# Kernel tuning notes

Hardware: AMD Instinct MI355X
Metric: run time of the kernel (lower is better)

Reference implementation:

```python
import jax, jax.numpy as jnp
import numpy as np

B, N, S, NS, D = 8, 16384, 1024, 64, 128
RADIUS = 0.2
CH = [131, 128, 128, 256]  # mlp_spec after use_xyz: 128+3 input channels
EPS = 1e-5


def setup_inputs() -> dict:
    key = jax.random.key(0)
    ks = jax.random.split(key, 16)
    inp = {}
    inp["xyz"] = jax.random.uniform(ks[0], (B, N, 3), dtype=jnp.float32)
    inp["points"] = jax.random.normal(ks[1], (B, D, N), dtype=jnp.float32)
    inp["fps_idx"] = jax.random.randint(ks[2], (B, S), 0, N, dtype=jnp.int32)
    for i in range(3):
        cin, cout = CH[i], CH[i + 1]
        inp[f"W{i}"] = jax.random.normal(ks[3 + 4 * i], (cout, cin), dtype=jnp.float32) * np.float32(1.0 / np.sqrt(cin))
        inp[f"b{i}"] = jnp.zeros((cout,), dtype=jnp.float32)
        inp[f"g{i}"] = jnp.ones((cout,), dtype=jnp.float32)
        inp[f"be{i}"] = jnp.zeros((cout,), dtype=jnp.float32)
    return inp


def _ball_query(xyz, new_xyz):
    # squared distances [B, S, N] (expanded-form, same math as square_distance)
    d = (jnp.sum(new_xyz ** 2, -1, keepdims=True)
         + jnp.sum(xyz ** 2, -1)[:, None, :]
         - 2.0 * jnp.einsum('bsc,bnc->bsn', new_xyz, xyz))
    ar = jnp.arange(N, dtype=jnp.int32)[None, None, :]
    idx = jnp.where(d > RADIUS ** 2, N, ar)          # out-of-ball -> sentinel N
    idx = jnp.sort(idx, axis=-1)[:, :, :NS]          # global sort emulating top-k
    idx = jnp.where(idx == N, idx[:, :, :1], idx)    # pad with first valid neighbor
    return idx


def reference(xyz, points, fps_idx, W0, b0, g0, be0, W1, b1, g1, be1, W2, b2, g2, be2):
    feats = points.transpose(0, 2, 1)  # [B, N, D]
    new_xyz = jnp.take_along_axis(xyz, fps_idx[..., None], axis=1)  # [B, S, 3]
    idx = _ball_query(xyz, new_xyz)  # [B, S, NS]

    gather = jax.vmap(lambda a, i: a[i])  # per-batch fancy gather
    grouped_xyz = gather(xyz, idx) - new_xyz[:, :, None, :]   # [B, S, NS, 3]
    grouped_pts = gather(feats, idx)                          # [B, S, NS, D]
    x = jnp.concatenate([grouped_xyz, grouped_pts], axis=-1)  # [B, S, NS, 131]

    # SharedMLP: 1x1 Conv2d + BatchNorm (training-mode stats) + ReLU
    for W, b, g, be in ((W0, b0, g0, be0), (W1, b1, g1, be1), (W2, b2, g2, be2)):
        x = jnp.einsum('bsnc,oc->bsno', x, W) + b
        m = jnp.mean(x, axis=(0, 1, 2))
        v = jnp.var(x, axis=(0, 1, 2))
        x = jax.nn.relu(g * (x - m) * jax.lax.rsqrt(v + EPS) + be)

    new_features = jnp.max(x, axis=2).transpose(0, 2, 1)  # max over nsample -> [B, C', S]
    return new_xyz, new_features, fps_idx
```

## Files before the change

kernel.cpp:

```cpp
#include <hip/hip_runtime.h>
#include <hip/hip_bf16.h>

#define BB 8
#define NN 16384
#define SS 1024
#define NSMP 64
#define DD 128
#define R2 0.04f
#define EPSV 1e-5f

typedef _Float16 half2t __attribute__((ext_vector_type(2)));
typedef _Float16 half8t __attribute__((ext_vector_type(8)));
typedef float f32x4 __attribute__((ext_vector_type(4)));

#define O_PT    0ull
#define O_Y0    33554432ull
#define O_Y1    167772160ull
#define O_IDX   301989888ull
#define O_MAXB  304087040ull
#define O_MINB  312475648ull
#define O_W0T   320864256ull
#define O_W1T   320931328ull
#define O_W2T   320996864ull
#define O_PS0   321127936ull
#define O_PQ0   321259008ull
#define O_PS1   321390080ull
#define O_PQ1   321521152ull
#define O_PS2   321652224ull
#define O_PQ2   321914368ull
#define O_SC0   322176512ull
#define O_SH0   322177024ull
#define O_SC1   322177536ull
#define O_SH1   322178048ull
#define O_SC2   322178560ull
#define O_SH2   322179584ull
#define WS_NEEDED 322180608ull
#define PART_BYTES 1048576ull

#define OUT_XYZ 0
#define OUT_FEAT 24576
#define OUT_FPS (24576 + 2097152)

__global__ __launch_bounds__(256) void k_transpose_pts(const float* __restrict__ pts,
                                                       _Float16* __restrict__ ptsT) {
  __shared__ float tile[32][33];
  int b = blockIdx.z;
  int n0 = blockIdx.x * 32, c0 = blockIdx.y * 32;
  int tx = threadIdx.x, ty = threadIdx.y;
#pragma unroll
  for (int k = 0; k < 4; k++) {
    int c = c0 + ty + k * 8;
    tile[ty + k * 8][tx] = pts[((size_t)b * DD + c) * NN + n0 + tx];
  }
  __syncthreads();
#pragma unroll
  for (int k = 0; k < 4; k++) {
    int n = n0 + ty + k * 8;
    ptsT[((size_t)b * NN + n) * DD + c0 + tx] = (_Float16)tile[tx][ty + k * 8];
  }
}

__global__ __launch_bounds__(256) void k_wt(const float* __restrict__ W0, const float* __restrict__ W1,
                                            const float* __restrict__ W2, _Float16* __restrict__ W0h,
                                            _Float16* __restrict__ W1h, _Float16* __restrict__ W2h) {
  int id = blockIdx.x * 256 + threadIdx.x;
  const int T0 = 128 * 136, T1 = 128 * 136, T2 = 256 * 136;
  if (id < T0) {
    int o = id / 136, c = id % 136;
    float v = 0.f;
    if (c < 131) {
      int c0 = (c < 128) ? (c + 3) : (c - 128);
      v = W0[o * 131 + c0];
    }
    W0h[id] = (_Float16)v;
  } else if (id < T0 + T1) {
    int j = id - T0;
    int o = j / 136, c = j % 136;
    W1h[j] = (_Float16)((c < 128) ? W1[o * 128 + c] : 0.f);
  } else if (id < T0 + T1 + T2) {
    int j = id - T0 - T1;
    int o = j / 136, c = j % 136;
    W2h[j] = (_Float16)((c < 128) ? W2[o * 128 + c] : 0.f);
  }
}

__global__ __launch_bounds__(256) void k_newxyz(const float* __restrict__ xyz, const int* __restrict__ fps,
                                                float* __restrict__ out) {
  int id = blockIdx.x * 256 + threadIdx.x;
  int fi = fps[id];
  int b = id >> 10;
  const float* p = xyz + ((size_t)b * NN + fi) * 3;
  float* o = out + OUT_XYZ + (size_t)id * 3;
  o[0] = p[0]; o[1] = p[1]; o[2] = p[2];
  out[OUT_FPS + id] = (float)fi;
}

__global__ __launch_bounds__(256) void k_ballq(const float* __restrict__ xyz, const int* __restrict__ fps,
                                               int* __restrict__ idxb) {
  int w = (blockIdx.x * 256 + threadIdx.x) >> 6;
  int lane = threadIdx.x & 63;
  int b = w >> 10;
  int fi = fps[w];
  const float* cp = xyz + ((size_t)b * NN + fi) * 3;
  float cx = cp[0], cy = cp[1], cz = cp[2];
  float A = __fadd_rn(__fadd_rn(__fmul_rn(cx, cx), __fmul_rn(cy, cy)), __fmul_rn(cz, cz));
  const float* xb = xyz + (size_t)b * NN * 3;
  int cnt = 0, firstn = -1;
  int* myidx = idxb + (size_t)w * NSMP;
  for (int nb = 0; nb < NN && cnt < NSMP; nb += 64) {
    int n = nb + lane;
    float px = xb[n * 3], py = xb[n * 3 + 1], pz = xb[n * 3 + 2];
    float Bv = __fadd_rn(__fadd_rn(__fmul_rn(px, px), __fmul_rn(py, py)), __fmul_rn(pz, pz));
    float dot = __fadd_rn(__fadd_rn(__fmul_rn(cx, px), __fmul_rn(cy, py)), __fmul_rn(cz, pz));
    float d = __fsub_rn(__fadd_rn(A, Bv), __fmul_rn(2.0f, dot));
    bool valid = !(d > R2);
    unsigned long long mask = __ballot(valid);
    if (firstn < 0 && mask) firstn = nb + __builtin_ctzll(mask);
    int prefix = __popcll(mask & ((1ull << lane) - 1ull));
    int pos = cnt + prefix;
    if (valid && pos < NSMP) myidx[pos] = n;
    cnt += __popcll(mask);
    if (cnt > NSMP) cnt = NSMP;
  }
  if (lane >= cnt) myidx[lane] = firstn;
}

__global__ __launch_bounds__(256, 2) void k_mlp0(const float* __restrict__ xyz,
                                                 const _Float16* __restrict__ ptsT,
                                                 const int* __restrict__ fps, const int* __restrict__ idxb,
                                                 const _Float16* __restrict__ W0h, const float* __restrict__ b0,
                                                 _Float16* __restrict__ y0, float* __restrict__ psum,
                                                 float* __restrict__ psq) {
  __shared__ _Float16 xh[64 * 136];
  __shared__ float xs[64 * 133];
  __shared__ float rbuf[128 * 2];
  __shared__ int smidx[64];
  __shared__ float smc[3];
  int t = threadIdx.x;
  int bs = blockIdx.x;
  int b = bs >> 10;
  if (t < 64) smidx[t] = idxb[(size_t)bs * 64 + t];
  if (t < 3) {
    int fi = fps[bs];
    smc[t] = xyz[((size_t)b * NN + fi) * 3 + t];
  }
  __syncthreads();
  {
    int row = t >> 2, q = t & 3;
    int n = smidx[row];
    const half8t* src = (const half8t*)(ptsT + ((size_t)b * NN + n) * DD);
#pragma unroll
    for (int i = 0; i < 4; i++) {
      int j = q + i * 4;
      *(half8t*)(xh + row * 136 + j * 8) = src[j];
    }
  }
  if (t < 64) {
    int n = smidx[t];
    const float* p = xyz + ((size_t)b * NN + n) * 3;
    xh[t * 136 + 128] = (_Float16)(p[0] - smc[0]);
    xh[t * 136 + 129] = (_Float16)(p[1] - smc[1]);
    xh[t * 136 + 130] = (_Float16)(p[2] - smc[2]);
  }
  __syncthreads();
  int lane = t & 63;
  int m0 = __builtin_amdgcn_readfirstlane((t >> 6) * 16);
  int lr = lane & 15, lk = lane >> 4;
  half8t afr[4];
#pragma unroll
  for (int kt = 0; kt < 4; kt++)
    afr[kt] = *(const half8t*)(xh + (m0 + lr) * 136 + kt * 32 + lk * 8);
  f32x4 acc[8];
#pragma unroll
  for (int nt = 0; nt < 8; nt++) {
    float bv = b0[nt * 16 + lr];
    f32x4 cv = {bv, bv, bv, bv};
    acc[nt] = cv;
  }
#pragma unroll
  for (int kt = 0; kt < 4; kt++) {
#pragma unroll
    for (int nt = 0; nt < 8; nt++) {
      half8t bw = *(const half8t*)(W0h + (nt * 16 + lr) * 136 + kt * 32 + lk * 8);
      acc[nt] = __builtin_amdgcn_mfma_f32_16x16x32_f16(afr[kt], bw, acc[nt], 0, 0, 0);
    }
  }
  {
    float xr[4][3];
#pragma unroll
    for (int r = 0; r < 4; r++) {
      int m = m0 + lk * 4 + r;
      xr[r][0] = (float)xh[m * 136 + 128];
      xr[r][1] = (float)xh[m * 136 + 129];
      xr[r][2] = (float)xh[m * 136 + 130];
    }
#pragma unroll
    for (int nt = 0; nt < 8; nt++) {
      const _Float16* wp = W0h + (nt * 16 + lr) * 136 + 128;
      float w0 = (float)wp[0], w1 = (float)wp[1], w2 = (float)wp[2];
#pragma unroll
      for (int r = 0; r < 4; r++)
        acc[nt][r] += xr[r][0] * w0 + xr[r][1] * w1 + xr[r][2] * w2;
    }
  }
#pragma unroll
  for (int nt = 0; nt < 8; nt++)
#pragma unroll
    for (int r = 0; r < 4; r++)
      xs[(m0 + lk * 4 + r) * 133 + nt * 16 + lr] = acc[nt][r];
  __syncthreads();
  {
    _Float16* dst = y0 + (size_t)bs * 8192;
#pragma unroll
    for (int i = 0; i < 16; i++) {
      int flat = i * 512 + 2 * t;
      int row = flat >> 7, col = flat & 127;
      half2t h;
      h[0] = (_Float16)xs[row * 133 + col];
      h[1] = (_Float16)xs[row * 133 + col + 1];
      *(half2t*)(dst + flat) = h;
    }
  }
  {
    int col = t & 127, half = t >> 7;
    float s = 0.f, q = 0.f;
#pragma unroll 4
    for (int r = half * 32; r < half * 32 + 32; r++) {
      float v = xs[r * 133 + col];
      s += v;
      q = fmaf(v, v, q);
    }
    if (half) { rbuf[col * 2] = s; rbuf[col * 2 + 1] = q; }
    __syncthreads();
    if (!half) {
      s += rbuf[col * 2];
      q += rbuf[col * 2 + 1];
      int slot = bs & 255;
      atomicAdd(&psum[col * 256 + slot], s);
      atomicAdd(&psq[col * 256 + slot], q);
    }
  }
}

__global__ __launch_bounds__(256, 2) void k_mlp1(const _Float16* __restrict__ y0,
                                                 const float* __restrict__ sc, const float* __restrict__ sh,
                                                 const _Float16* __restrict__ W1h, const float* __restrict__ b1,
                                                 _Float16* __restrict__ y1, float* __restrict__ psum,
                                                 float* __restrict__ psq) {
  __shared__ _Float16 xh[64 * 136];
  __shared__ float xs[64 * 133];
  __shared__ float rbuf[128 * 2];
  int t = threadIdx.x;
  int bs = blockIdx.x;
  {
    int colb = (2 * t) & 127;
    float a0 = sc[colb], a1 = sc[colb + 1];
    float c0 = sh[colb], c1 = sh[colb + 1];
    const _Float16* src = y0 + (size_t)bs * 8192;
#pragma unroll
    for (int i = 0; i < 16; i++) {
      int flat = i * 512 + 2 * t;
      int row = flat >> 7, col = flat & 127;
      half2t h = *(const half2t*)(src + flat);
      half2t o;
      o[0] = (_Float16)fmaxf(fmaf((float)h[0], a0, c0), 0.f);
      o[1] = (_Float16)fmaxf(fmaf((float)h[1], a1, c1), 0.f);
      *(half2t*)(xh + row * 136 + col) = o;
    }
  }
  __syncthreads();
  int lane = t & 63;
  int m0 = __builtin_amdgcn_readfirstlane((t >> 6) * 16);
  int lr = lane & 15, lk = lane >> 4;
  half8t afr[4];
#pragma unroll
  for (int kt = 0; kt < 4; kt++)
    afr[kt] = *(const half8t*)(xh + (m0 + lr) * 136 + kt * 32 + lk * 8);
  f32x4 acc[8];
#pragma unroll
  for (int nt = 0; nt < 8; nt++) {
    float bv = b1[nt * 16 + lr];
    f32x4 cv = {bv, bv, bv, bv};
    acc[nt] = cv;
  }
#pragma unroll
  for (int kt = 0; kt < 4; kt++) {
#pragma unroll
    for (int nt = 0; nt < 8; nt++) {
      half8t bw = *(const half8t*)(W1h + (nt * 16 + lr) * 136 + kt * 32 + lk * 8);
      acc[nt] = __builtin_amdgcn_mfma_f32_16x16x32_f16(afr[kt], bw, acc[nt], 0, 0, 0);
    }
  }
#pragma unroll
  for (int nt = 0; nt < 8; nt++)
#pragma unroll
    for (int r = 0; r < 4; r++)
      xs[(m0 + lk * 4 + r) * 133 + nt * 16 + lr] = acc[nt][r];
  __syncthreads();
  {
    _Float16* dst = y1 + (size_t)bs * 8192;
#pragma unroll
    for (int i = 0; i < 16; i++) {
      int flat = i * 512 + 2 * t;
      int row = flat >> 7, col = flat & 127;
      half2t h;
      h[0] = (_Float16)xs[row * 133 + col];
      h[1] = (_Float16)xs[row * 133 + col + 1];
      *(half2t*)(dst + flat) = h;
    }
  }
  {
    int col = t & 127, half = t >> 7;
    float s = 0.f, q = 0.f;
#pragma unroll 4
    for (int r = half * 32; r < half * 32 + 32; r++) {
      float v = xs[r * 133 + col];
      s += v;
      q = fmaf(v, v, q);
    }
    if (half) { rbuf[col * 2] = s; rbuf[col * 2 + 1] = q; }
    __syncthreads();
    if (!half) {
      s += rbuf[col * 2];
      q += rbuf[col * 2 + 1];
      int slot = bs & 255;
      atomicAdd(&psum[col * 256 + slot], s);
      atomicAdd(&psq[col * 256 + slot], q);
    }
  }
}

__global__ __launch_bounds__(256, 2) void k_mlp2(const _Float16* __restrict__ y1,
                                                 const float* __restrict__ sc, const float* __restrict__ sh,
                                                 const _Float16* __restrict__ W2h, const float* __restrict__ b2,
                                                 float* __restrict__ maxb, float* __restrict__ minb,
                                                 float* __restrict__ psum, float* __restrict__ psq) {
  __shared__ _Float16 xh[64 * 136];
  __shared__ float xs[64 * 133];
  __shared__ float rbuf[128 * 4];
  int t = threadIdx.x;
  int bs = blockIdx.x;
  {
    int colb = (2 * t) & 127;
    float a0 = sc[colb], a1 = sc[colb + 1];
    float c0 = sh[colb], c1 = sh[colb + 1];
    const _Float16* src = y1 + (size_t)bs * 8192;
#pragma unroll
    for (int i = 0; i < 16; i++) {
      int flat = i * 512 + 2 * t;
      int row = flat >> 7, col = flat & 127;
      half2t h = *(const half2t*)(src + flat);
      half2t o;
      o[0] = (_Float16)fmaxf(fmaf((float)h[0], a0, c0), 0.f);
      o[1] = (_Float16)fmaxf(fmaf((float)h[1], a1, c1), 0.f);
      *(half2t*)(xh + row * 136 + col) = o;
    }
  }
  __syncthreads();
  int lane = t & 63;
  int m0 = __builtin_amdgcn_readfirstlane((t >> 6) * 16);
  int lr = lane & 15, lk = lane >> 4;
  half8t afr[4];
#pragma unroll
  for (int kt = 0; kt < 4; kt++)
    afr[kt] = *(const half8t*)(xh + (m0 + lr) * 136 + kt * 32 + lk * 8);
  f32x4 acc[16];
#pragma unroll
  for (int nt = 0; nt < 16; nt++) {
    float bv = b2[nt * 16 + lr];
    f32x4 cv = {bv, bv, bv, bv};
    acc[nt] = cv;
  }
#pragma unroll
  for (int kt = 0; kt < 4; kt++) {
#pragma unroll
    for (int nt = 0; nt < 16; nt++) {
      half8t bw = *(const half8t*)(W2h + (nt * 16 + lr) * 136 + kt * 32 + lk * 8);
      acc[nt] = __builtin_amdgcn_mfma_f32_16x16x32_f16(afr[kt], bw, acc[nt], 0, 0, 0);
    }
  }
  for (int ph = 0; ph < 2; ph++) {
#pragma unroll
    for (int nt = 0; nt < 8; nt++)
#pragma unroll
      for (int r = 0; r < 4; r++)
        xs[(m0 + lk * 4 + r) * 133 + nt * 16 + lr] = acc[ph * 8 + nt][r];
    __syncthreads();
    {
      int col = t & 127, half = t >> 7;
      float s = 0.f, q = 0.f, mx = -3.4e38f, mn = 3.4e38f;
#pragma unroll 4
      for (int r = half * 32; r < half * 32 + 32; r++) {
        float v = xs[r * 133 + col];
        s += v;
        q = fmaf(v, v, q);
        mx = fmaxf(mx, v);
        mn = fminf(mn, v);
      }
      if (half) {
        rbuf[col * 4] = s; rbuf[col * 4 + 1] = q;
        rbuf[col * 4 + 2] = mx; rbuf[col * 4 + 3] = mn;
      }
      __syncthreads();
      if (!half) {
        s += rbuf[col * 4];
        q += rbuf[col * 4 + 1];
        mx = fmaxf(mx, rbuf[col * 4 + 2]);
        mn = fminf(mn, rbuf[col * 4 + 3]);
        int o = ph * 128 + col;
        maxb[(size_t)bs * 256 + o] = mx;
        minb[(size_t)bs * 256 + o] = mn;
        int slot = bs & 255;
        atomicAdd(&psum[o * 256 + slot], s);
        atomicAdd(&psq[o * 256 + slot], q);
      }
    }
    __syncthreads();
  }
}

__global__ __launch_bounds__(256) void k_fin(const float* __restrict__ psum, const float* __restrict__ psq,
                                             const float* __restrict__ g, const float* __restrict__ be,
                                             float* __restrict__ sc, float* __restrict__ sh, int nch) {
  int o = threadIdx.x;
  if (o >= nch) return;
  float s = 0.f, q = 0.f;
  for (int k = 0; k < 256; k++) {
    s += psum[o * 256 + k];
    q += psq[o * 256 + k];
  }
  const float inv = 1.0f / 524288.0f;
  float m = s * inv;
  float ey2 = q * inv;
  float v = fmaf(-m, m, ey2);
  v = fmaxf(v, 0.f);
  float r = rsqrtf(v + EPSV);
  float a = g[o] * r;
  sc[o] = a;
  sh[o] = fmaf(-m, a, be[o]);
}

__global__ __launch_bounds__(256) void k_out(const float* __restrict__ maxb, const float* __restrict__ minb,
                                             const float* __restrict__ sc, const float* __restrict__ sh,
                                             float* __restrict__ out) {
  int flat = blockIdx.x * 256 + threadIdx.x;
  int b = flat >> 18;
  int o = (flat >> 10) & 255;
  int s = flat & 1023;
  float a = sc[o], c_ = sh[o];
  size_t mi = ((size_t)(b * 1024 + s)) * 256 + o;
  float v = (a >= 0.f) ? maxb[mi] : minb[mi];
  out[OUT_FEAT + flat] = fmaxf(fmaf(a, v, c_), 0.f);
}

extern "C" void kernel_launch(void* const* d_in, const int* in_sizes, int n_in,
                              void* d_out, int out_size, void* d_ws, size_t ws_size,
                              hipStream_t stream) {
  const float* xyz = (const float*)d_in[0];
  const float* pts = (const float*)d_in[1];
  const int* fps = (const int*)d_in[2];
  const float* W0 = (const float*)d_in[3];
  const float* b0 = (const float*)d_in[4];
  const float* g0 = (const float*)d_in[5];
  const float* be0 = (const float*)d_in[6];
  const float* W1 = (const float*)d_in[7];
  const float* b1 = (const float*)d_in[8];
  const float* g1 = (const float*)d_in[9];
  const float* be1 = (const float*)d_in[10];
  const float* W2 = (const float*)d_in[11];
  const float* b2 = (const float*)d_in[12];
  const float* g2 = (const float*)d_in[13];
  const float* be2 = (const float*)d_in[14];
  float* out = (float*)d_out;
  char* ws = (char*)d_ws;

  k_newxyz<<<32, 256, 0, stream>>>(xyz, fps, out);
  if (ws_size < WS_NEEDED) return;

  _Float16* ptsT = (_Float16*)(ws + O_PT);
  _Float16* y0 = (_Float16*)(ws + O_Y0);
  _Float16* y1 = (_Float16*)(ws + O_Y1);
  int* idxb = (int*)(ws + O_IDX);
  float* maxbf = (float*)(ws + O_MAXB);
  float* minbf = (float*)(ws + O_MINB);
  _Float16* W0h = (_Float16*)(ws + O_W0T);
  _Float16* W1h = (_Float16*)(ws + O_W1T);
  _Float16* W2h = (_Float16*)(ws + O_W2T);
  float* ps0 = (float*)(ws + O_PS0);
  float* pq0 = (float*)(ws + O_PQ0);
  float* ps1 = (float*)(ws + O_PS1);
  float* pq1 = (float*)(ws + O_PQ1);
  float* ps2 = (float*)(ws + O_PS2);
  float* pq2 = (float*)(ws + O_PQ2);
  float* sc0 = (float*)(ws + O_SC0);
  float* sh0 = (float*)(ws + O_SH0);
  float* sc1 = (float*)(ws + O_SC1);
  float* sh1 = (float*)(ws + O_SH1);
  float* sc2 = (float*)(ws + O_SC2);
  float* sh2 = (float*)(ws + O_SH2);

  hipMemsetAsync(ws + O_PS0, 0, PART_BYTES, stream);
  k_transpose_pts<<<dim3(NN / 32, DD / 32, BB), dim3(32, 8), 0, stream>>>(pts, ptsT);
  k_wt<<<272, 256, 0, stream>>>(W0, W1, W2, W0h, W1h, W2h);
  k_ballq<<<2048, 256, 0, stream>>>(xyz, fps, idxb);
  k_mlp0<<<8192, 256, 0, stream>>>(xyz, ptsT, fps, idxb, W0h, b0, y0, ps0, pq0);
  k_fin<<<1, 256, 0, stream>>>(ps0, pq0, g0, be0, sc0, sh0, 128);
  k_mlp1<<<8192, 256, 0, stream>>>(y0, sc0, sh0, W1h, b1, y1, ps1, pq1);
  k_fin<<<1, 256, 0, stream>>>(ps1, pq1, g1, be1, sc1, sh1, 128);
  k_mlp2<<<8192, 256, 0, stream>>>(y1, sc1, sh1, W2h, b2, maxbf, minbf, ps2, pq2);
  k_fin<<<1, 256, 0, stream>>>(ps2, pq2, g2, be2, sc2, sh2, 256);
  k_out<<<8192, 256, 0, stream>>>(maxbf, minbf, sc2, sh2, out);
}
```

Baseline: 116.8 us.

## Recompute earlier MLP layers per pass instead of storing fp16 intermediates

Replaces the three layer kernels, which wrote and re-read the fp16 activations y0 and y1 through global memory, with three passes that each re-gather the ball features and recompute the earlier layers in registers and LDS. Only per-channel stats, and max/min in the final pass, are written. This removes about 256MB of activation traffic at the cost of repeating the gather and the layer-0/1 MFMA work. It also folds the partial-sum zeroing into the weight-conversion kernel in place of a memset, and writes new_xyz/fps from the ball-query kernel so the separate newxyz launch goes away.

After: 114.3 us. 2.1% less time.

```diff
diff --git a/kernel.cpp b/kernel.cpp
--- a/kernel.cpp
+++ b/kernel.cpp
@@ -14,8 +14,6 @@
 typedef float f32x4 __attribute__((ext_vector_type(4)));
 
 #define O_PT    0ull
-#define O_Y0    33554432ull
-#define O_Y1    167772160ull
 #define O_IDX   301989888ull
 #define O_MAXB  304087040ull
 #define O_MINB  312475648ull
@@ -35,7 +33,6 @@
 #define O_SC2   322178560ull
 #define O_SH2   322179584ull
 #define WS_NEEDED 322180608ull
-#define PART_BYTES 1048576ull
 
 #define OUT_XYZ 0
 #define OUT_FEAT 24576
@@ -62,8 +59,13 @@
 
 __global__ __launch_bounds__(256) void k_wt(const float* __restrict__ W0, const float* __restrict__ W1,
                                             const float* __restrict__ W2, _Float16* __restrict__ W0h,
-                                            _Float16* __restrict__ W1h, _Float16* __restrict__ W2h) {
+                                            _Float16* __restrict__ W1h, _Float16* __restrict__ W2h,
+                                            float* __restrict__ zreg) {
   int id = blockIdx.x * 256 + threadIdx.x;
+  if (id < 65536) {
+    f32x4 z = {0.f, 0.f, 0.f, 0.f};
+    ((f32x4*)zreg)[id] = z;
+  }
   const int T0 = 128 * 136, T1 = 128 * 136, T2 = 256 * 136;
   if (id < T0) {
     int o = id / 136, c = id % 136;
@@ -96,13 +98,15 @@
 }
 
 __global__ __launch_bounds__(256) void k_ballq(const float* __restrict__ xyz, const int* __restrict__ fps,
-                                               int* __restrict__ idxb) {
+                                               int* __restrict__ idxb, float* __restrict__ out) {
   int w = (blockIdx.x * 256 + threadIdx.x) >> 6;
   int lane = threadIdx.x & 63;
   int b = w >> 10;
   int fi = fps[w];
   const float* cp = xyz + ((size_t)b * NN + fi) * 3;
   float cx = cp[0], cy = cp[1], cz = cp[2];
+  if (lane < 3) out[OUT_XYZ + (size_t)w * 3 + lane] = (lane == 0) ? cx : ((lane == 1) ? cy : cz);
+  if (lane == 3) out[OUT_FPS + w] = (float)fi;
   float A = __fadd_rn(__fadd_rn(__fmul_rn(cx, cx), __fmul_rn(cy, cy)), __fmul_rn(cz, cz));
   const float* xb = xyz + (size_t)b * NN * 3;
   int cnt = 0, firstn = -1;
@@ -125,12 +129,151 @@
   if (lane >= cnt) myidx[lane] = firstn;
 }
 
-__global__ __launch_bounds__(256, 2) void k_mlp0(const float* __restrict__ xyz,
-                                                 const _Float16* __restrict__ ptsT,
-                                                 const int* __restrict__ fps, const int* __restrict__ idxb,
-                                                 const _Float16* __restrict__ W0h, const float* __restrict__ b0,
-                                                 _Float16* __restrict__ y0, float* __restrict__ psum,
-                                                 float* __restrict__ psq) {
+
+__device__ __forceinline__ void load_ball(const float* __restrict__ xyz,
+                                          const _Float16* __restrict__ ptsT,
+                                          const int* __restrict__ fps, const int* __restrict__ idxb,
+                                          int bs, int b, int t, _Float16* xh, int* smidx, float* smc) {
+  if (t < 64) smidx[t] = idxb[(size_t)bs * 64 + t];
+  if (t < 3) {
+    int fi = fps[bs];
+    smc[t] = xyz[((size_t)b * NN + fi) * 3 + t];
+  }
+  __syncthreads();
+  {
+    int row = t >> 2, q = t & 3;
+    int n = smidx[row];
+    const half8t* src = (const half8t*)(ptsT + ((size_t)b * NN + n) * DD);
+#pragma unroll
+    for (int i = 0; i < 4; i++) {
+      int j = q + i * 4;
+      *(half8t*)(xh + row * 136 + j * 8) = src[j];
+    }
+  }
+  if (t < 64) {
+    int n = smidx[t];
+    const float* p = xyz + ((size_t)b * NN + n) * 3;
+    xh[t * 136 + 128] = (_Float16)(p[0] - smc[0]);
+    xh[t * 136 + 129] = (_Float16)(p[1] - smc[1]);
+    xh[t * 136 + 130] = (_Float16)(p[2] - smc[2]);
+  }
+  __syncthreads();
+}
+
+__device__ __forceinline__ void mfma_l0(const _Float16* xh, const _Float16* __restrict__ W0h,
+                                        const float* __restrict__ b0, int m0, int lr, int lk,
+                                        f32x4* acc) {
+  half8t afr[4];
+#pragma unroll
+  for (int kt = 0; kt < 4; kt++)
+    afr[kt] = *(const half8t*)(xh + (m0 + lr) * 136 + kt * 32 + lk * 8);
+#pragma unroll
+  for (int nt = 0; nt < 8; nt++) {
+    float bv = b0[nt * 16 + lr];
+    f32x4 cv = {bv, bv, bv, bv};
+    acc[nt] = cv;
+  }
+#pragma unroll
+  for (int kt = 0; kt < 4; kt++) {
+#pragma unroll
+    for (int nt = 0; nt < 8; nt++) {
+      half8t bw = *(const half8t*)(W0h + (nt * 16 + lr) * 136 + kt * 32 + lk * 8);
+      acc[nt] = __builtin_amdgcn_mfma_f32_16x16x32_f16(afr[kt], bw, acc[nt], 0, 0, 0);
+    }
+  }
+  float xr[4][3];
+#pragma unroll
+  for (int r = 0; r < 4; r++) {
+    int m = m0 + lk * 4 + r;
+    xr[r][0] = (float)xh[m * 136 + 128];
+    xr[r][1] = (float)xh[m * 136 + 129];
+    xr[r][2] = (float)xh[m * 136 + 130];
+  }
+#pragma unroll
+  for (int nt = 0; nt < 8; nt++) {
+    const _Float16* wp = W0h + (nt * 16 + lr) * 136 + 128;
+    float w0 = (float)wp[0], w1 = (float)wp[1], w2 = (float)wp[2];
+#pragma unroll
+    for (int r = 0; r < 4; r++)
+      acc[nt][r] += xr[r][0] * w0 + xr[r][1] * w1 + xr[r][2] * w2;
+  }
+}
+
+template <int NT>
+__device__ __forceinline__ void mfma_lx(const _Float16* xh, const _Float16* __restrict__ Wh,
+                                        const float* __restrict__ bias, int m0, int lr, int lk,
+                                        f32x4* acc) {
+  half8t afr[4];
+#pragma unroll
+  for (int kt = 0; kt < 4; kt++)
+    afr[kt] = *(const half8t*)(xh + (m0 + lr) * 136 + kt * 32 + lk * 8);
+#pragma unroll
+  for (int nt = 0; nt < NT; nt++) {
+    float bv = bias[nt * 16 + lr];
+    f32x4 cv = {bv, bv, bv, bv};
+    acc[nt] = cv;
+  }
+#pragma unroll
+  for (int kt = 0; kt < 4; kt++) {
+#pragma unroll
+    for (int nt = 0; nt < NT; nt++) {
+      half8t bw = *(const half8t*)(Wh + (nt * 16 + lr) * 136 + kt * 32 + lk * 8);
+      acc[nt] = __builtin_amdgcn_mfma_f32_16x16x32_f16(afr[kt], bw, acc[nt], 0, 0, 0);
+    }
+  }
+}
+
+__device__ __forceinline__ void store_act(_Float16* xh, const float* __restrict__ sc,
+                                          const float* __restrict__ sh, int m0, int lr, int lk,
+                                          const f32x4* acc) {
+#pragma unroll
+  for (int nt = 0; nt < 8; nt++) {
+    int col = nt * 16 + lr;
+    float a = sc[col], c = sh[col];
+#pragma unroll
+    for (int r = 0; r < 4; r++) {
+      float v = fmaxf(fmaf(acc[nt][r], a, c), 0.f);
+      xh[(m0 + lk * 4 + r) * 136 + col] = (_Float16)v;
+    }
+  }
+}
+
+__device__ __forceinline__ void dump_xs(float* xs, const f32x4* acc, int m0, int lr, int lk) {
+#pragma unroll
+  for (int nt = 0; nt < 8; nt++)
+#pragma unroll
+    for (int r = 0; r < 4; r++)
+      xs[(m0 + lk * 4 + r) * 133 + nt * 16 + lr] = acc[nt][r];
+}
+
+__device__ __forceinline__ void stats_epilogue(const float* xs, float* rbuf,
+                                               float* __restrict__ psum, float* __restrict__ psq,
+                                               int t, int bs) {
+  int col = t & 127, hf = t >> 7;
+  float s = 0.f, q = 0.f;
+#pragma unroll 4
+  for (int r = hf * 32; r < hf * 32 + 32; r++) {
+    float v = xs[r * 133 + col];
+    s += v;
+    q = fmaf(v, v, q);
+  }
+  if (hf) { rbuf[col * 2] = s; rbuf[col * 2 + 1] = q; }
+  __syncthreads();
+  if (!hf) {
+    s += rbuf[col * 2];
+    q += rbuf[col * 2 + 1];
+    int slot = bs & 255;
+    atomicAdd(&psum[col * 256 + slot], s);
+    atomicAdd(&psq[col * 256 + slot], q);
+  }
+}
+
+
+__global__ __launch_bounds__(256, 2) void k_pass1(const float* __restrict__ xyz,
+                                                  const _Float16* __restrict__ ptsT,
+                                                  const int* __restrict__ fps, const int* __restrict__ idxb,
+                                                  const _Float16* __restrict__ W0h, const float* __restrict__ b0,
+                                                  float* __restrict__ psum, float* __restrict__ psq) {
   __shared__ _Float16 xh[64 * 136];
   __shared__ float xs[64 * 133];
   __shared__ float rbuf[128 * 2];
@@ -139,270 +282,104 @@
   int t = threadIdx.x;
   int bs = blockIdx.x;
   int b = bs >> 10;
-  if (t < 64) smidx[t] = idxb[(size_t)bs * 64 + t];
-  if (t < 3) {
-    int fi = fps[bs];
-    smc[t] = xyz[((size_t)b * NN + fi) * 3 + t];
-  }
-  __syncthreads();
-  {
-    int row = t >> 2, q = t & 3;
-    int n = smidx[row];
-    const half8t* src = (const half8t*)(ptsT + ((size_t)b * NN + n) * DD);
-#pragma unroll
-    for (int i = 0; i < 4; i++) {
-      int j = q + i * 4;
-      *(half8t*)(xh + row * 136 + j * 8) = src[j];
-    }
-  }
-  if (t < 64) {
-    int n = smidx[t];
-    const float* p = xyz + ((size_t)b * NN + n) * 3;
-    xh[t * 136 + 128] = (_Float16)(p[0] - smc[0]);
-    xh[t * 136 + 129] = (_Float16)(p[1] - smc[1]);
-    xh[t * 136 + 130] = (_Float16)(p[2] - smc[2]);
-  }
-  __syncthreads();
+  load_ball(xyz, ptsT, fps, idxb, bs, b, t, xh, smidx, smc);
   int lane = t & 63;
   int m0 = __builtin_amdgcn_readfirstlane((t >> 6) * 16);
   int lr = lane & 15, lk = lane >> 4;
-  half8t afr[4];
-#pragma unroll
-  for (int kt = 0; kt < 4; kt++)
-    afr[kt] = *(const half8t*)(xh + (m0 + lr) * 136 + kt * 32 + lk * 8);
   f32x4 acc[8];
-#pragma unroll
-  for (int nt = 0; nt < 8; nt++) {
-    float bv = b0[nt * 16 + lr];
-    f32x4 cv = {bv, bv, bv, bv};
-    acc[nt] = cv;
-  }
-#pragma unroll
-  for (int kt = 0; kt < 4; kt++) {
-#pragma unroll
-    for (int nt = 0; nt < 8; nt++) {
-      half8t bw = *(const half8t*)(W0h + (nt * 16 + lr) * 136 + kt * 32 + lk * 8);
-      acc[nt] = __builtin_amdgcn_mfma_f32_16x16x32_f16(afr[kt], bw, acc[nt], 0, 0, 0);
-    }
-  }
-  {
-    float xr[4][3];
-#pragma unroll
-    for (int r = 0; r < 4; r++) {
-      int m = m0 + lk * 4 + r;
-      xr[r][0] = (float)xh[m * 136 + 128];
-      xr[r][1] = (float)xh[m * 136 + 129];
-      xr[r][2] = (float)xh[m * 136 + 130];
-    }
-#pragma unroll
-    for (int nt = 0; nt < 8; nt++) {
-      const _Float16* wp = W0h + (nt * 16 + lr) * 136 + 128;
-      float w0 = (float)wp[0], w1 = (float)wp[1], w2 = (float)wp[2];
-#pragma unroll
-      for (int r = 0; r < 4; r++)
-        acc[nt][r] += xr[r][0] * w0 + xr[r][1] * w1 + xr[r][2] * w2;
-    }
-  }
-#pragma unroll
-  for (int nt = 0; nt < 8; nt++)
-#pragma unroll
-    for (int r = 0; r < 4; r++)
-      xs[(m0 + lk * 4 + r) * 133 + nt * 16 + lr] = acc[nt][r];
-  __syncthreads();
-  {
-    _Float16* dst = y0 + (size_t)bs * 8192;
-#pragma unroll
-    for (int i = 0; i < 16; i++) {
-      int flat = i * 512 + 2 * t;
-      int row = flat >> 7, col = flat & 127;
-      half2t h;
-      h[0] = (_Float16)xs[row * 133 + col];
-      h[1] = (_Float16)xs[row * 133 + col + 1];
-      *(half2t*)(dst + flat) = h;
-    }
-  }
-  {
-    int col = t & 127, half = t >> 7;
-    float s = 0.f, q = 0.f;
-#pragma unroll 4
-    for (int r = half * 32; r < half * 32 + 32; r++) {
-      float v = xs[r * 133 + col];
-      s += v;
-      q = fmaf(v, v, q);
-    }
-    if (half) { rbuf[col * 2] = s; rbuf[col * 2 + 1] = q; }
-    __syncthreads();
-    if (!half) {
-      s += rbuf[col * 2];
-      q += rbuf[col * 2 + 1];
-      int slot = bs & 255;
-      atomicAdd(&psum[col * 256 + slot], s);
-      atomicAdd(&psq[col * 256 + slot], q);
-    }
-  }
-}
-
-__global__ __launch_bounds__(256, 2) void k_mlp1(const _Float16* __restrict__ y0,
-                                                 const float* __restrict__ sc, const float* __restrict__ sh,
-                                                 const _Float16* __restrict__ W1h, const float* __restrict__ b1,
-                                                 _Float16* __restrict__ y1, float* __restrict__ psum,
-                                                 float* __restrict__ psq) {
+  mfma_l0(xh, W0h, b0, m0, lr, lk, acc);
+  dump_xs(xs, acc, m0, lr, lk);
+  __syncthreads();
+  stats_epilogue(xs, rbuf, psum, psq, t, bs);
+}
+
+__global__ __launch_bounds__(256, 2) void k_pass2(const float* __restrict__ xyz,
+                                                  const _Float16* __restrict__ ptsT,
+                                                  const int* __restrict__ fps, const int* __restrict__ idxb,
+                                                  const _Float16* __restrict__ W0h, const float* __restrict__ b0,
+                                                  const float* __restrict__ sc0, const float* __restrict__ sh0,
+                                                  const _Float16* __restrict__ W1h, const float* __restrict__ b1,
+                                                  float* __restrict__ psum, float* __restrict__ psq) {
   __shared__ _Float16 xh[64 * 136];
   __shared__ float xs[64 * 133];
   __shared__ float rbuf[128 * 2];
+  __shared__ int smidx[64];
+  __shared__ float smc[3];
   int t = threadIdx.x;
   int bs = blockIdx.x;
-  {
-    int colb = (2 * t) & 127;
-    float a0 = sc[colb], a1 = sc[colb + 1];
-    float c0 = sh[colb], c1 = sh[colb + 1];
-    const _Float16* src = y0 + (size_t)bs * 8192;
-#pragma unroll
-    for (int i = 0; i < 16; i++) {
-      int flat = i * 512 + 2 * t;
-      int row = flat >> 7, col = flat & 127;
-      half2t h = *(const half2t*)(src + flat);
-      half2t o;
-      o[0] = (_Float16)fmaxf(fmaf((float)h[0], a0, c0), 0.f);
-      o[1] = (_Float16)fmaxf(fmaf((float)h[1], a1, c1), 0.f);
-      *(half2t*)(xh + row * 136 + col) = o;
-    }
-  }
-  __syncthreads();
+  int b = bs >> 10;
+  load_ball(xyz, ptsT, fps, idxb, bs, b, t, xh, smidx, smc);
   int lane = t & 63;
   int m0 = __builtin_amdgcn_readfirstlane((t >> 6) * 16);
   int lr = lane & 15, lk = lane >> 4;
-  half8t afr[4];
-#pragma unroll
-  for (int kt = 0; kt < 4; kt++)
-    afr[kt] = *(const half8t*)(xh + (m0 + lr) * 136 + kt * 32 + lk * 8);
   f32x4 acc[8];
-#pragma unroll
-  for (int nt = 0; nt < 8; nt++) {
-    float bv = b1[nt * 16 + lr];
-    f32x4 cv = {bv, bv, bv, bv};
-    acc[nt] = cv;
-  }
-#pragma unroll
-  for (int kt = 0; kt < 4; kt++) {
-#pragma unroll
-    for (int nt = 0; nt < 8; nt++) {
-      half8t bw = *(const half8t*)(W1h + (nt * 16 + lr) * 136 + kt * 32 + lk * 8);
-      acc[nt] = __builtin_amdgcn_mfma_f32_16x16x32_f16(afr[kt], bw, acc[nt], 0, 0, 0);
-    }
-  }
-#pragma unroll
-  for (int nt = 0; nt < 8; nt++)
-#pragma unroll
-    for (int r = 0; r < 4; r++)
-      xs[(m0 + lk * 4 + r) * 133 + nt * 16 + lr] = acc[nt][r];
-  __syncthreads();
-  {
-    _Float16* dst = y1 + (size_t)bs * 8192;
-#pragma unroll
-    for (int i = 0; i < 16; i++) {
-      int flat = i * 512 + 2 * t;
-      int row = flat >> 7, col = flat & 127;
-      half2t h;
-      h[0] = (_Float16)xs[row * 133 + col];
-      h[1] = (_Float16)xs[row * 133 + col + 1];
-      *(half2t*)(dst + flat) = h;
-    }
-  }
-  {
-    int col = t & 127, half = t >> 7;
-    float s = 0.f, q = 0.f;
-#pragma unroll 4
-    for (int r = half * 32; r < half * 32 + 32; r++) {
-      float v = xs[r * 133 + col];
-      s += v;
-      q = fmaf(v, v, q);
-    }
-    if (half) { rbuf[col * 2] = s; rbuf[col * 2 + 1] = q; }
-    __syncthreads();
-    if (!half) {
-      s += rbuf[col * 2];
-      q += rbuf[col * 2 + 1];
-      int slot = bs & 255;
-      atomicAdd(&psum[col * 256 + slot], s);
-      atomicAdd(&psq[col * 256 + slot], q);
-    }
-  }
-}
-
-__global__ __launch_bounds__(256, 2) void k_mlp2(const _Float16* __restrict__ y1,
-                                                 const float* __restrict__ sc, const float* __restrict__ sh,
-                                                 const _Float16* __restrict__ W2h, const float* __restrict__ b2,
-                                                 float* __restrict__ maxb, float* __restrict__ minb,
-                                                 float* __restrict__ psum, float* __restrict__ psq) {
+  mfma_l0(xh, W0h, b0, m0, lr, lk, acc);
+  __syncthreads();
+  store_act(xh, sc0, sh0, m0, lr, lk, acc);
+  __syncthreads();
+  mfma_lx<8>(xh, W1h, b1, m0, lr, lk, acc);
+  dump_xs(xs, acc, m0, lr, lk);
+  __syncthreads();
+  stats_epilogue(xs, rbuf, psum, psq, t, bs);
+}
+
+__global__ __launch_bounds__(256, 2) void k_pass3(const float* __restrict__ xyz,
+                                                  const _Float16* __restrict__ ptsT,
+                                                  const int* __restrict__ fps, const int* __restrict__ idxb,
+                                                  const _Float16* __restrict__ W0h, const float* __restrict__ b0,
+                                                  const float* __restrict__ sc0, const float* __restrict__ sh0,
+                                                  const _Float16* __restrict__ W1h, const float* __restrict__ b1,
+                                                  const float* __restrict__ sc1, const float* __restrict__ sh1,
+                                                  const _Float16* __restrict__ W2h, const float* __restrict__ b2,
+                                                  float* __restrict__ maxb, float* __restrict__ minb,
+                                                  float* __restrict__ psum, float* __restrict__ psq) {
   __shared__ _Float16 xh[64 * 136];
   __shared__ float xs[64 * 133];
   __shared__ float rbuf[128 * 4];
+  __shared__ int smidx[64];
+  __shared__ float smc[3];
   int t = threadIdx.x;
   int bs = blockIdx.x;
-  {
-    int colb = (2 * t) & 127;
-    float a0 = sc[colb], a1 = sc[colb + 1];
-    float c0 = sh[colb], c1 = sh[colb + 1];
-    const _Float16* src = y1 + (size_t)bs * 8192;
-#pragma unroll
-    for (int i = 0; i < 16; i++) {
-      int flat = i * 512 + 2 * t;
-      int row = flat >> 7, col = flat & 127;
-      half2t h = *(const half2t*)(src + flat);
-      half2t o;
-      o[0] = (_Float16)fmaxf(fmaf((float)h[0], a0, c0), 0.f);
-      o[1] = (_Float16)fmaxf(fmaf((float)h[1], a1, c1), 0.f);
-      *(half2t*)(xh + row * 136 + col) = o;
-    }
-  }
-  __syncthreads();
+  int b = bs >> 10;
+  load_ball(xyz, ptsT, fps, idxb, bs, b, t, xh, smidx, smc);
   int lane = t & 63;
   int m0 = __builtin_amdgcn_readfirstlane((t >> 6) * 16);
   int lr = lane & 15, lk = lane >> 4;
-  half8t afr[4];
-#pragma unroll
-  for (int kt = 0; kt < 4; kt++)
-    afr[kt] = *(const half8t*)(xh + (m0 + lr) * 136 + kt * 32 + lk * 8);
-  f32x4 acc[16];
-#pragma unroll
-  for (int nt = 0; nt < 16; nt++) {
-    float bv = b2[nt * 16 + lr];
-    f32x4 cv = {bv, bv, bv, bv};
-    acc[nt] = cv;
-  }
-#pragma unroll
-  for (int kt = 0; kt < 4; kt++) {
-#pragma unroll
-    for (int nt = 0; nt < 16; nt++) {
-      half8t bw = *(const half8t*)(W2h + (nt * 16 + lr) * 136 + kt * 32 + lk * 8);
-      acc[nt] = __builtin_amdgcn_mfma_f32_16x16x32_f16(afr[kt], bw, acc[nt], 0, 0, 0);
-    }
-  }
+  f32x4 acc[8];
+  mfma_l0(xh, W0h, b0, m0, lr, lk, acc);
+  __syncthreads();
+  store_act(xh, sc0, sh0, m0, lr, lk, acc);
+  __syncthreads();
+  mfma_lx<8>(xh, W1h, b1, m0, lr, lk, acc);
+  __syncthreads();
+  store_act(xh, sc1, sh1, m0, lr, lk, acc);
+  __syncthreads();
+  f32x4 acc2[16];
+  mfma_lx<16>(xh, W2h, b2, m0, lr, lk, acc2);
   for (int ph = 0; ph < 2; ph++) {
 #pragma unroll
     for (int nt = 0; nt < 8; nt++)
 #pragma unroll
       for (int r = 0; r < 4; r++)
-        xs[(m0 + lk * 4 + r) * 133 + nt * 16 + lr] = acc[ph * 8 + nt][r];
+        xs[(m0 + lk * 4 + r) * 133 + nt * 16 + lr] = acc2[ph * 8 + nt][r];
     __syncthreads();
     {
-      int col = t & 127, half = t >> 7;
+      int col = t & 127, hf = t >> 7;
       float s = 0.f, q = 0.f, mx = -3.4e38f, mn = 3.4e38f;
 #pragma unroll 4
-      for (int r = half * 32; r < half * 32 + 32; r++) {
+      for (int r = hf * 32; r < hf * 32 + 32; r++) {
         float v = xs[r * 133 + col];
         s += v;
         q = fmaf(v, v, q);
         mx = fmaxf(mx, v);
         mn = fminf(mn, v);
       }
-      if (half) {
+      if (hf) {
         rbuf[col * 4] = s; rbuf[col * 4 + 1] = q;
         rbuf[col * 4 + 2] = mx; rbuf[col * 4 + 3] = mn;
       }
       __syncthreads();
-      if (!half) {
+      if (!hf) {
         s += rbuf[col * 4];
         q += rbuf[col * 4 + 1];
         mx = fmaxf(mx, rbuf[col * 4 + 2]);
@@ -474,12 +451,12 @@
   float* out = (float*)d_out;
   char* ws = (char*)d_ws;
 
-  k_newxyz<<<32, 256, 0, stream>>>(xyz, fps, out);
-  if (ws_size < WS_NEEDED) return;
+  if (ws_size < WS_NEEDED) {
+    k_newxyz<<<32, 256, 0, stream>>>(xyz, fps, out);
+    return;
+  }
 
   _Float16* ptsT = (_Float16*)(ws + O_PT);
-  _Float16* y0 = (_Float16*)(ws + O_Y0);
-  _Float16* y1 = (_Float16*)(ws + O_Y1);
   int* idxb = (int*)(ws + O_IDX);
   float* maxbf = (float*)(ws + O_MAXB);
   float* minbf = (float*)(ws + O_MINB);
@@ -499,15 +476,15 @@
   float* sc2 = (float*)(ws + O_SC2);
   float* sh2 = (float*)(ws + O_SH2);
 
-  hipMemsetAsync(ws + O_PS0, 0, PART_BYTES, stream);
   k_transpose_pts<<<dim3(NN / 32, DD / 32, BB), dim3(32, 8), 0, stream>>>(pts, ptsT);
-  k_wt<<<272, 256, 0, stream>>>(W0, W1, W2, W0h, W1h, W2h);
-  k_ballq<<<2048, 256, 0, stream>>>(xyz, fps, idxb);
-  k_mlp0<<<8192, 256, 0, stream>>>(xyz, ptsT, fps, idxb, W0h, b0, y0, ps0, pq0);
+  k_wt<<<272, 256, 0, stream>>>(W0, W1, W2, W0h, W1h, W2h, ps0);
+  k_ballq<<<2048, 256, 0, stream>>>(xyz, fps, idxb, out);
+  k_pass1<<<8192, 256, 0, stream>>>(xyz, ptsT, fps, idxb, W0h, b0, ps0, pq0);
   k_fin<<<1, 256, 0, stream>>>(ps0, pq0, g0, be0, sc0, sh0, 128);
-  k_mlp1<<<8192, 256, 0, stream>>>(y0, sc0, sh0, W1h, b1, y1, ps1, pq1);
+  k_pass2<<<8192, 256, 0, stream>>>(xyz, ptsT, fps, idxb, W0h, b0, sc0, sh0, W1h, b1, ps1, pq1);
   k_fin<<<1, 256, 0, stream>>>(ps1, pq1, g1, be1, sc1, sh1, 128);
-  k_mlp2<<<8192, 256, 0, stream>>>(y1, sc1, sh1, W2h, b2, maxbf, minbf, ps2, pq2);
+  k_pass3<<<8192, 256, 0, stream>>>(xyz, ptsT, fps, idxb, W0h, b0, sc0, sh0, W1h, b1, sc1, sh1,
+                                    W2h, b2, maxbf, minbf, ps2, pq2);
   k_fin<<<1, 256, 0, stream>>>(ps2, pq2, g2, be2, sc2, sh2, 256);
   k_out<<<8192, 256, 0, stream>>>(maxbf, minbf, sc2, sh2, out);
 }
```
